# Kernel tuning notes

Measured on AMD Instinct MI355X. Metric: run time of the kernel, lower is better.

The kernel has to match this reference:

```python
import jax, jax.numpy as jnp
import numpy as np

LN_EPS = 1e-5
NEG_INF = -1e38


def wkv_scan(w, u, k, v):
    """Numerically-stable RWKV WKV recurrence (matches wkv_cuda forward).
    w: [C] (negative decay), u: [C] bonus, k/v: [B,T,C]. Returns y: [B,T,C]."""
    Bdim, T, C = k.shape

    def step(carry, kv_t):
        p, q, o = carry  # running num, den, log-scale, each [B,C]
        kt, vt = kv_t
        no = jnp.maximum(o, u + kt)
        A = jnp.exp(o - no)
        Bw = jnp.exp(u + kt - no)
        y = (A * p + Bw * vt) / (A * q + Bw)
        no2 = jnp.maximum(w + o, kt)
        A2 = jnp.exp(w + o - no2)
        B2 = jnp.exp(kt - no2)
        return (A2 * p + B2 * vt, A2 * q + B2, no2), y

    init = (jnp.zeros((Bdim, C), k.dtype), jnp.zeros((Bdim, C), k.dtype),
            jnp.full((Bdim, C), NEG_INF, k.dtype))
    kT = jnp.moveaxis(k, 1, 0)  # [T,B,C]
    vT = jnp.moveaxis(v, 1, 0)
    _, ys = jax.lax.scan(step, init, (kT, vT))
    return jnp.moveaxis(ys, 0, 1)  # [B,T,C]


def setup_inputs() -> dict:
    key = jax.random.key(0)
    ks = jax.random.split(key, 8)
    B, C, H, W = 16, 192, 56, 56
    s = 0.02
    x = jax.random.normal(ks[0], (B, C, H, W), jnp.float32)
    Wk = jax.random.normal(ks[1], (C, C), jnp.float32) * s
    Wv = jax.random.normal(ks[2], (C, C), jnp.float32) * s
    Wr = jax.random.normal(ks[3], (C, C), jnp.float32) * s
    Wo = jax.random.normal(ks[4], (C, C), jnp.float32) * s
    ln_g = jnp.ones((C,), jnp.float32)
    ln_b = jnp.zeros((C,), jnp.float32)
    w_decay = -6.0 + 0.1 * jax.random.normal(ks[5], (C,), jnp.float32)
    u = 0.1 * jax.random.normal(ks[6], (C,), jnp.float32)
    return {"x": x, "Wk": Wk, "Wv": Wv, "Wr": Wr, "Wo": Wo,
            "ln_g": ln_g, "ln_b": ln_b, "w_decay": w_decay, "u": u}


def reference(x, Wk, Wv, Wr, Wo, ln_g, ln_b, w_decay, u):
    B, C, H, W = x.shape
    xs = jnp.transpose(x.reshape(B, C, H * W), (0, 2, 1))  # [B,T,C]
    k = jnp.einsum('btc,dc->btd', xs, Wk)
    v = jnp.einsum('btc,dc->btd', xs, Wv)
    r = jnp.einsum('btc,dc->btd', xs, Wr)
    real_w = -jnp.exp(w_decay)
    x_fwd = wkv_scan(real_w, u, k, v)
    x_bwd = jnp.flip(wkv_scan(real_w, u, jnp.flip(k, 1), jnp.flip(v, 1)), 1)
    x_bi = 0.5 * (x_fwd + x_bwd)
    h = jax.nn.sigmoid(r) * x_bi
    mu = jnp.mean(h, axis=-1, keepdims=True)
    var = jnp.var(h, axis=-1, keepdims=True)
    h = (h - mu) * jax.lax.rsqrt(var + LN_EPS) * ln_g + ln_b
    out = jnp.einsum('btc,dc->btd', h, Wo)  # dropout is identity at eval
    return jnp.transpose(out, (0, 2, 1)).reshape(B, C, H, W)
```

## Files before the change

### kernel.cpp

```cpp
#include <hip/hip_runtime.h>
#include <hip/hip_bf16.h>

#define BB 16
#define CC 192
#define TPIX 3136
#define NCH 49
#define CHL 64
#define NNELE ((size_t)BB * TPIX * CC)
#define NSTATE ((size_t)2 * BB * NCH * CC)
#define WCH (CC * CC)

typedef __attribute__((ext_vector_type(8))) short bf16x8;
typedef __attribute__((ext_vector_type(4))) float f32x4;
typedef __attribute__((ext_vector_type(16))) float f32x16;

__device__ __forceinline__ unsigned short f2bf(float f) {
    __hip_bfloat16 b = __float2bfloat16(f);
    return *reinterpret_cast<unsigned short*>(&b);
}
__device__ __forceinline__ float bf2f(unsigned short h) {
    union { unsigned u; float f; } v; v.u = ((unsigned)h) << 16;
    return v.f;
}


__global__ __launch_bounds__(256) void wcvt_frag(
    const float* __restrict__ Wk, const float* __restrict__ Wv,
    const float* __restrict__ Wr, const float* __restrict__ Wo,
    unsigned short* __restrict__ wfrag)
{
    const int id = blockIdx.x * 256 + threadIdx.x;
    const int m = id / 4608;
    const int r = id % 4608;
    const int tile = r >> 6;
    const int lane = r & 63;
    const int dr = tile / 12, tk = tile % 12;
    const int d = dr * 32 + (lane & 31);
    const int c = tk * 16 + (lane >> 5) * 8;
    const float* W = (m == 0) ? Wk : (m == 1) ? Wv : (m == 2) ? Wr : Wo;
    const float4 a = *(const float4*)&W[d * CC + c];
    const float4 b = *(const float4*)&W[d * CC + c + 4];
    bf16x8 o;
    o[0] = (short)f2bf(a.x); o[1] = (short)f2bf(a.y);
    o[2] = (short)f2bf(a.z); o[3] = (short)f2bf(a.w);
    o[4] = (short)f2bf(b.x); o[5] = (short)f2bf(b.y);
    o[6] = (short)f2bf(b.z); o[7] = (short)f2bf(b.w);
    *(bf16x8*)&wfrag[(size_t)m * WCH + (size_t)tile * 512 + lane * 8] = o;
}

__global__ __launch_bounds__(256) void xcvt_frag(
    const float* __restrict__ x, unsigned short* __restrict__ xfrag)
{
    const int t0 = blockIdx.x * 32;
    const int b  = blockIdx.y;
    __shared__ float ls[CC][33];
    const int tid = threadIdx.x;
#pragma unroll
    for (int it = 0; it < 6; ++it) {
        const int c  = it * 32 + (tid >> 3);
        const int t4 = (tid & 7) * 4;
        *(float4*)&ls[c][t4] =
            *(const float4*)&x[((size_t)b * CC + c) * TPIX + t0 + t4];
    }
    __syncthreads();
    const size_t tbase = ((size_t)(b * TPIX + t0) >> 5) * 12;
#pragma unroll
    for (int it = 0; it < 3; ++it) {
        const int id = it * 256 + tid;
        const int tk = id >> 6;
        const int lane = id & 63;
        const int r32 = lane & 31;
        const int c0 = tk * 16 + (lane >> 5) * 8;
        bf16x8 o;
#pragma unroll
        for (int e = 0; e < 8; ++e)
            o[e] = (short)f2bf(ls[c0 + e][r32]);
        *(bf16x8*)&xfrag[(tbase + tk) * 512 + lane * 8] = o;
    }
}

__global__ __launch_bounds__(512, 4) void proj_mfma32(
    const unsigned short* __restrict__ xfrag,
    const unsigned short* __restrict__ wfrag,
    unsigned short* __restrict__ kbf, unsigned short* __restrict__ vbf,
    unsigned short* __restrict__ rfrag)
{
    __shared__ unsigned short wlds[WCH];
    const int tid  = threadIdx.x;
    const int lane = tid & 63;
    const int wv   = tid >> 6;
    const int tw   = wv >> 1;
    const int dwav = wv & 1;
    const int l31  = lane & 31;
    const int kh   = lane >> 5;
    const int m    = blockIdx.z;

    const size_t row0 = (size_t)blockIdx.x * 128 + tw * 32;
    const size_t xtb  = (row0 >> 5) * 12;

    bf16x8 xf[12];
#pragma unroll
    for (int ks = 0; ks < 12; ++ks)
        xf[ks] = *(const bf16x8*)&xfrag[(xtb + ks) * 512 + lane * 8];

    const unsigned short* wm = wfrag + (size_t)m * WCH;
#pragma unroll
    for (int it = 0; it < 9; ++it) {
        const int off = (it * 512 + tid) * 8;
        *(bf16x8*)&wlds[off] = *(const bf16x8*)&wm[off];
    }
    __syncthreads();

    f32x16 acc[3];
#pragma unroll
    for (int nn = 0; nn < 3; ++nn)
#pragma unroll
        for (int e = 0; e < 16; ++e) acc[nn][e] = 0.f;

#pragma unroll
    for (int ks = 0; ks < 12; ++ks) {
        bf16x8 wf[3];
#pragma unroll
        for (int nn = 0; nn < 3; ++nn)
            wf[nn] = *(const bf16x8*)&wlds[((dwav * 3 + nn) * 12 + ks) * 512 + lane * 8];
#pragma unroll
        for (int nn = 0; nn < 3; ++nn)
            acc[nn] = __builtin_amdgcn_mfma_f32_32x32x16_bf16(
                xf[ks], wf[nn], acc[nn], 0, 0, 0);
    }

    if (m == 2) {
#pragma unroll
        for (int nn = 0; nn < 3; ++nn) {
            const int d = dwav * 96 + nn * 32 + l31;
            const size_t tb = ((row0 >> 5) * 12 + (d >> 4)) * 512 +
                              (size_t)(((d >> 3) & 1) * 32) * 8 + (d & 7);
#pragma unroll
            for (int q = 0; q < 16; ++q) {
                const int tq = (q & 3) + 8 * (q >> 2) + 4 * kh;
                rfrag[tb + tq * 8] = f2bf(acc[nn][q]);
            }
        }
    } else {
        unsigned short* om = (m == 0) ? kbf : vbf;
#pragma unroll
        for (int nn = 0; nn < 3; ++nn) {
            const int d = dwav * 96 + nn * 32 + l31;
#pragma unroll
            for (int q = 0; q < 16; ++q) {
                const int t = (q & 3) + 8 * (q >> 2) + 4 * kh;
                om[(row0 + t) * CC + d] = f2bf(acc[nn][q]);
            }
        }
    }
}

__global__ __launch_bounds__(256) void wkv_chunk_kernel(
    const unsigned short* __restrict__ kb, const unsigned short* __restrict__ vb,
    const float* __restrict__ wdec,
    float* __restrict__ sp, float* __restrict__ sq, float* __restrict__ so)
{
    const int gid = blockIdx.x * 256 + threadIdx.x;
    const int c  = gid % CC;
    const int r  = gid / CC;
    const int ch = r % NCH;
    const int r2 = r / NCH;
    const int b  = r2 % BB;
    const int dir = r2 / BB;

    const float w = -__expf(wdec[c]);
    const int tstart = dir ? (TPIX - 1 - ch * CHL) : (ch * CHL);
    const long stride = dir ? -(long)CC : (long)CC;
    long idx = ((long)b * TPIX + tstart) * CC + c;

    float p = 0.f, q = 0.f, o = -1e38f;
#pragma unroll 4
    for (int j = 0; j < CHL; ++j) {
        const float kt = bf2f(kb[idx]), vt = bf2f(vb[idx]);
        const float wo  = w + o;
        const float no2 = fmaxf(wo, kt);
        const float A2  = __expf(wo - no2);
        const float B2  = __expf(kt - no2);
        p = A2 * p + B2 * vt;
        q = A2 * q + B2;
        o = no2;
        idx += stride;
    }
    sp[gid] = p; sq[gid] = q; so[gid] = o;
}

__global__ __launch_bounds__(256) void wkv_prefix_kernel(
    float* __restrict__ sp, float* __restrict__ sq, float* __restrict__ so,
    const float* __restrict__ wdec)
{
    const int tid = blockIdx.x * 256 + threadIdx.x;
    if (tid >= 2 * BB * CC) return;
    const int c = tid % CC;
    const int g = tid / CC;
    const float w  = -__expf(wdec[c]);
    const float wL = w * CHL;

    float P = 0.f, Q = 0.f, O = -1e38f;
    size_t idx = (size_t)g * NCH * CC + c;
    for (int ch = 0; ch < NCH; ++ch) {
        const float pl = sp[idx], ql = sq[idx], ol = so[idx];
        sp[idx] = P; sq[idx] = Q; so[idx] = O;
        const float Ow = O + wL;
        const float no = fmaxf(Ow, ol);
        const float A  = __expf(Ow - no);
        const float Bf = __expf(ol - no);
        P = A * P + Bf * pl;
        Q = A * Q + Bf * ql;
        O = no;
        idx += CC;
    }
}

__global__ __launch_bounds__(256) void wkv_emit_kernel(
    const unsigned short* __restrict__ kb, const unsigned short* __restrict__ vb,
    const float* __restrict__ wdec, const float* __restrict__ ubias,
    const float* __restrict__ sp, const float* __restrict__ sq,
    const float* __restrict__ so,
    unsigned short* __restrict__ yfwd, unsigned short* __restrict__ ybwd)
{
    const int gid = blockIdx.x * 256 + threadIdx.x;
    const int c  = gid % CC;
    const int r  = gid / CC;
    const int ch = r % NCH;
    const int r2 = r / NCH;
    const int b  = r2 % BB;
    const int dir = r2 / BB;

    const float w = -__expf(wdec[c]);
    const float u = ubias[c];
    const int tstart = dir ? (TPIX - 1 - ch * CHL) : (ch * CHL);
    const long stride = dir ? -(long)CC : (long)CC;
    const int rstep = dir ? -1 : 1;
    long idx = ((long)b * TPIX + tstart) * CC + c;
    long row = (long)b * TPIX + tstart;
    unsigned short* yout = dir ? ybwd : yfwd;
    const int ctile = c >> 4;
    const int clane = ((c >> 3) & 1) * 32;
    const int ce    = c & 7;

    float p = sp[gid], q = sq[gid], o = so[gid];
#pragma unroll 2
    for (int j = 0; j < CHL; ++j) {
        const float kt = bf2f(kb[idx]), vt = bf2f(vb[idx]);
        const float uk  = u + kt;
        const float no  = fmaxf(o, uk);
        const float A   = __expf(o - no);
        const float Bw  = __expf(uk - no);
        const float num = A * p + Bw * vt;
        const float den = A * q + Bw;
        const size_t off = ((size_t)(row >> 5) * 12 + ctile) * 512 +
                           (size_t)((row & 31) + clane) * 8 + ce;
        yout[off] = f2bf(0.5f * __fdividef(num, den));
        const float wo  = w + o;
        const float no2 = fmaxf(wo, kt);
        const float A2  = __expf(wo - no2);
        const float B2  = __expf(kt - no2);
        p = A2 * p + B2 * vt;
        q = A2 * q + B2;
        o = no2;
        idx += stride;
        row += rstep;
    }
}

__global__ __launch_bounds__(512, 2) void outproj_ln_mfma32(
    const unsigned short* __restrict__ yfwd, const unsigned short* __restrict__ ybwd,
    const unsigned short* __restrict__ rfrag,
    const float* __restrict__ gamma, const float* __restrict__ beta,
    const unsigned short* __restrict__ wo,
    float* __restrict__ out)
{
    __shared__ unsigned short wlds[WCH];
    __shared__ float gblds[CC];
    __shared__ float bblds[CC];
    const int tid  = threadIdx.x;
    const int lane = tid & 63;
    const int wv   = tid >> 6;
    const int tw   = wv >> 1;
    const int dwav = wv & 1;
    const int l31  = lane & 31;
    const int kh   = lane >> 5;

#pragma unroll
    for (int it = 0; it < 9; ++it) {
        const int off = (it * 512 + tid) * 8;
        *(bf16x8*)&wlds[off] = *(const bf16x8*)&wo[off];
    }
    if (tid < CC) { gblds[tid] = gamma[tid]; bblds[tid] = beta[tid]; }
    __syncthreads();

    const size_t row0 = (size_t)blockIdx.x * 128 + tw * 32;
    const size_t htb  = (row0 >> 5) * 12;

    bf16x8 hvb[12];
    float s = 0.f, s2 = 0.f;
#pragma unroll
    for (int ks = 0; ks < 12; ++ks) {
        const size_t fo = (htb + ks) * 512 + lane * 8;
        const bf16x8 yf = *(const bf16x8*)&yfwd[fo];
        const bf16x8 yb = *(const bf16x8*)&ybwd[fo];
        const bf16x8 rv = *(const bf16x8*)&rfrag[fo];
        bf16x8 hb;
#pragma unroll
        for (int e = 0; e < 8; ++e) {
            const float xb = bf2f((unsigned short)yf[e]) + bf2f((unsigned short)yb[e]);
            const float rr = bf2f((unsigned short)rv[e]);
            const float h  = xb / (1.f + __expf(-rr));
            s += h; s2 += h * h;
            hb[e] = (short)f2bf(h);
        }
        hvb[ks] = hb;
    }
    s  += __shfl_xor(s, 32);
    s2 += __shfl_xor(s2, 32);
    const float mu   = s * (1.f / CC);
    const float var  = s2 * (1.f / CC) - mu * mu;
    const float rstd = rsqrtf(var + 1e-5f);

#pragma unroll
    for (int ks = 0; ks < 12; ++ks) {
        const int cbase = ks * 16 + kh * 8;
        bf16x8 hb = hvb[ks];
#pragma unroll
        for (int e = 0; e < 8; ++e) {
            const float h = (bf2f((unsigned short)hb[e]) - mu) * rstd *
                            gblds[cbase + e] + bblds[cbase + e];
            hb[e] = (short)f2bf(h);
        }
        hvb[ks] = hb;
    }

    f32x16 acc[3];
#pragma unroll
    for (int nn = 0; nn < 3; ++nn)
#pragma unroll
        for (int e = 0; e < 16; ++e) acc[nn][e] = 0.f;

#pragma unroll
    for (int ks = 0; ks < 12; ++ks) {
        bf16x8 wf[3];
#pragma unroll
        for (int nn = 0; nn < 3; ++nn)
            wf[nn] = *(const bf16x8*)&wlds[((dwav * 3 + nn) * 12 + ks) * 512 + lane * 8];
#pragma unroll
        for (int nn = 0; nn < 3; ++nn)
            acc[nn] = __builtin_amdgcn_mfma_f32_32x32x16_bf16(
                hvb[ks], wf[nn], acc[nn], 0, 0, 0);
    }

#pragma unroll
    for (int nn = 0; nn < 3; ++nn) {
        const int d = dwav * 96 + nn * 32 + l31;
#pragma unroll
        for (int q2 = 0; q2 < 4; ++q2) {
            const size_t grow = row0 + 4 * kh + 8 * q2;
            const int b  = (int)(grow / TPIX);
            const int tl = (int)(grow % TPIX);
            f32x4 v4 = {acc[nn][q2 * 4 + 0], acc[nn][q2 * 4 + 1],
                        acc[nn][q2 * 4 + 2], acc[nn][q2 * 4 + 3]};
            *(f32x4*)&out[((size_t)b * CC + d) * TPIX + tl] = v4;
        }
    }
}

extern "C" void kernel_launch(void* const* d_in, const int* in_sizes, int n_in,
                              void* d_out, int out_size, void* d_ws, size_t ws_size,
                              hipStream_t stream)
{
    const float* x    = (const float*)d_in[0];
    const float* Wk   = (const float*)d_in[1];
    const float* Wv   = (const float*)d_in[2];
    const float* Wr   = (const float*)d_in[3];
    const float* Wo   = (const float*)d_in[4];
    const float* ln_g = (const float*)d_in[5];
    const float* ln_b = (const float*)d_in[6];
    const float* wdec = (const float*)d_in[7];
    const float* u    = (const float*)d_in[8];

    unsigned short* kbf   = (unsigned short*)d_ws;
    unsigned short* vbf   = kbf + NNELE;
    unsigned short* rfrag = vbf + NNELE;
    unsigned short* xfrag = rfrag + NNELE;
    unsigned short* wfrag = xfrag + NNELE;
    unsigned short* yfwd  = wfrag + 4 * WCH;
    unsigned short* ybwd  = yfwd + NNELE;
    float* sp = (float*)xfrag;
    float* sq = sp + NSTATE;
    float* so = sq + NSTATE;
    float* out = (float*)d_out;

    wcvt_frag<<<72, 256, 0, stream>>>(Wk, Wv, Wr, Wo, wfrag);
    xcvt_frag<<<dim3(TPIX / 32, BB), 256, 0, stream>>>(x, xfrag);

    proj_mfma32<<<dim3((BB * TPIX) / 128, 1, 3), 512, 0, stream>>>(
        xfrag, wfrag, kbf, vbf, rfrag);

    const int nth = (int)NSTATE;
    wkv_chunk_kernel<<<nth / 256, 256, 0, stream>>>(kbf, vbf, wdec, sp, sq, so);
    wkv_prefix_kernel<<<(2 * BB * CC + 255) / 256, 256, 0, stream>>>(sp, sq, so, wdec);
    wkv_emit_kernel<<<nth / 256, 256, 0, stream>>>(kbf, vbf, wdec, u, sp, sq, so, yfwd, ybwd);

    outproj_ln_mfma32<<<(BB * TPIX) / 128, 512, 0, stream>>>(
        yfwd, ybwd, rfrag, ln_g, ln_b, wfrag + 3 * WCH, out);
}
```

Baseline: 132.2 us.

## Fold LayerNorm into output projection via gamma-scaled weights and MFMA row sums

Rewrites LayerNorm plus the output projection algebraically. Gamma is folded into the bf16 Wo fragments, and Wo·gamma and Wo·beta are precomputed in a small new kernel. Per-row mean and variance are computed by extra MFMAs against a ones vector, and normalization is applied after the GEMM, so h is no longer held across two passes. This removes the 12-register-vector hvb buffer and the second normalization loop. In exchange it adds two extra MFMAs per k-step and an extra launch, and it computes variance from bf16-rounded h² via E[x²]-mu², which risks cancellation error. It also drops the min-2-blocks occupancy hint.

New measurement: 136.0 us. +2.8%, slower.

```diff
diff --git a/kernel.cpp b/kernel.cpp
--- a/kernel.cpp
+++ b/kernel.cpp
@@ -9,6 +9,7 @@
 #define NNELE ((size_t)BB * TPIX * CC)
 #define NSTATE ((size_t)2 * BB * NCH * CC)
 #define WCH (CC * CC)
+#define NROWS ((size_t)BB * TPIX)
 
 typedef __attribute__((ext_vector_type(8))) short bf16x8;
 typedef __attribute__((ext_vector_type(4))) float f32x4;
@@ -27,6 +28,7 @@
 __global__ __launch_bounds__(256) void wcvt_frag(
     const float* __restrict__ Wk, const float* __restrict__ Wv,
     const float* __restrict__ Wr, const float* __restrict__ Wo,
+    const float* __restrict__ gamma,
     unsigned short* __restrict__ wfrag)
 {
     const int id = blockIdx.x * 256 + threadIdx.x;
@@ -40,12 +42,32 @@
     const float* W = (m == 0) ? Wk : (m == 1) ? Wv : (m == 2) ? Wr : Wo;
     const float4 a = *(const float4*)&W[d * CC + c];
     const float4 b = *(const float4*)&W[d * CC + c + 4];
+    float g[8];
+#pragma unroll
+    for (int i = 0; i < 8; ++i) g[i] = (m == 3) ? gamma[c + i] : 1.f;
     bf16x8 o;
-    o[0] = (short)f2bf(a.x); o[1] = (short)f2bf(a.y);
-    o[2] = (short)f2bf(a.z); o[3] = (short)f2bf(a.w);
-    o[4] = (short)f2bf(b.x); o[5] = (short)f2bf(b.y);
-    o[6] = (short)f2bf(b.z); o[7] = (short)f2bf(b.w);
+    o[0] = (short)f2bf(a.x * g[0]); o[1] = (short)f2bf(a.y * g[1]);
+    o[2] = (short)f2bf(a.z * g[2]); o[3] = (short)f2bf(a.w * g[3]);
+    o[4] = (short)f2bf(b.x * g[4]); o[5] = (short)f2bf(b.y * g[5]);
+    o[6] = (short)f2bf(b.z * g[6]); o[7] = (short)f2bf(b.w * g[7]);
     *(bf16x8*)&wfrag[(size_t)m * WCH + (size_t)tile * 512 + lane * 8] = o;
+}
+
+__global__ __launch_bounds__(192) void wgb_kernel(
+    const float* __restrict__ Wo, const float* __restrict__ gamma,
+    const float* __restrict__ beta,
+    float* __restrict__ Wg, float* __restrict__ Wb)
+{
+    const int d = threadIdx.x;
+    float sg = 0.f, sb = 0.f;
+    for (int c = 0; c < CC; c += 4) {
+        const float4 w = *(const float4*)&Wo[d * CC + c];
+        const float4 g = *(const float4*)&gamma[c];
+        const float4 bb = *(const float4*)&beta[c];
+        sg += w.x * g.x + w.y * g.y + w.z * g.z + w.w * g.w;
+        sb += w.x * bb.x + w.y * bb.y + w.z * bb.z + w.w * bb.w;
+    }
+    Wg[d] = sg; Wb[d] = sb;
 }
 
 __global__ __launch_bounds__(256) void xcvt_frag(
@@ -268,16 +290,14 @@
     }
 }
 
-__global__ __launch_bounds__(512, 2) void outproj_ln_mfma32(
+__global__ __launch_bounds__(512) void outproj_ln_mfma32(
     const unsigned short* __restrict__ yfwd, const unsigned short* __restrict__ ybwd,
     const unsigned short* __restrict__ rfrag,
-    const float* __restrict__ gamma, const float* __restrict__ beta,
+    const float* __restrict__ Wg, const float* __restrict__ Wb,
     const unsigned short* __restrict__ wo,
     float* __restrict__ out)
 {
     __shared__ unsigned short wlds[WCH];
-    __shared__ float gblds[CC];
-    __shared__ float bblds[CC];
     const int tid  = threadIdx.x;
     const int lane = tid & 63;
     const int wv   = tid >> 6;
@@ -286,63 +306,43 @@
     const int l31  = lane & 31;
     const int kh   = lane >> 5;
 
+    const size_t row0 = (size_t)blockIdx.x * 128 + tw * 32;
+    const size_t htb  = (row0 >> 5) * 12;
+
 #pragma unroll
     for (int it = 0; it < 9; ++it) {
         const int off = (it * 512 + tid) * 8;
         *(bf16x8*)&wlds[off] = *(const bf16x8*)&wo[off];
     }
-    if (tid < CC) { gblds[tid] = gamma[tid]; bblds[tid] = beta[tid]; }
     __syncthreads();
 
-    const size_t row0 = (size_t)blockIdx.x * 128 + tw * 32;
-    const size_t htb  = (row0 >> 5) * 12;
-
-    bf16x8 hvb[12];
-    float s = 0.f, s2 = 0.f;
+    bf16x8 ones;
+#pragma unroll
+    for (int e = 0; e < 8; ++e) ones[e] = (short)0x3F80;
+
+    f32x16 acc[3], accs, accs2;
+#pragma unroll
+    for (int nn = 0; nn < 3; ++nn)
+#pragma unroll
+        for (int e = 0; e < 16; ++e) acc[nn][e] = 0.f;
+#pragma unroll
+    for (int e = 0; e < 16; ++e) { accs[e] = 0.f; accs2[e] = 0.f; }
+
 #pragma unroll
     for (int ks = 0; ks < 12; ++ks) {
         const size_t fo = (htb + ks) * 512 + lane * 8;
         const bf16x8 yf = *(const bf16x8*)&yfwd[fo];
         const bf16x8 yb = *(const bf16x8*)&ybwd[fo];
         const bf16x8 rv = *(const bf16x8*)&rfrag[fo];
-        bf16x8 hb;
+        bf16x8 hb, hq;
 #pragma unroll
         for (int e = 0; e < 8; ++e) {
             const float xb = bf2f((unsigned short)yf[e]) + bf2f((unsigned short)yb[e]);
             const float rr = bf2f((unsigned short)rv[e]);
-            const float h  = xb / (1.f + __expf(-rr));
-            s += h; s2 += h * h;
+            const float h  = __fdividef(xb, 1.f + __expf(-rr));
             hb[e] = (short)f2bf(h);
+            hq[e] = (short)f2bf(h * h);
         }
-        hvb[ks] = hb;
-    }
-    s  += __shfl_xor(s, 32);
-    s2 += __shfl_xor(s2, 32);
-    const float mu   = s * (1.f / CC);
-    const float var  = s2 * (1.f / CC) - mu * mu;
-    const float rstd = rsqrtf(var + 1e-5f);
-
-#pragma unroll
-    for (int ks = 0; ks < 12; ++ks) {
-        const int cbase = ks * 16 + kh * 8;
-        bf16x8 hb = hvb[ks];
-#pragma unroll
-        for (int e = 0; e < 8; ++e) {
-            const float h = (bf2f((unsigned short)hb[e]) - mu) * rstd *
-                            gblds[cbase + e] + bblds[cbase + e];
-            hb[e] = (short)f2bf(h);
-        }
-        hvb[ks] = hb;
-    }
-
-    f32x16 acc[3];
-#pragma unroll
-    for (int nn = 0; nn < 3; ++nn)
-#pragma unroll
-        for (int e = 0; e < 16; ++e) acc[nn][e] = 0.f;
-
-#pragma unroll
-    for (int ks = 0; ks < 12; ++ks) {
         bf16x8 wf[3];
 #pragma unroll
         for (int nn = 0; nn < 3; ++nn)
@@ -350,19 +350,36 @@
 #pragma unroll
         for (int nn = 0; nn < 3; ++nn)
             acc[nn] = __builtin_amdgcn_mfma_f32_32x32x16_bf16(
-                hvb[ks], wf[nn], acc[nn], 0, 0, 0);
+                hb, wf[nn], acc[nn], 0, 0, 0);
+        accs  = __builtin_amdgcn_mfma_f32_32x32x16_bf16(hb, ones, accs, 0, 0, 0);
+        accs2 = __builtin_amdgcn_mfma_f32_32x32x16_bf16(hq, ones, accs2, 0, 0, 0);
+    }
+
+    float muv[16], rsv[16];
+#pragma unroll
+    for (int q = 0; q < 16; ++q) {
+        const float mu  = accs[q] * (1.f / CC);
+        const float var = accs2[q] * (1.f / CC) - mu * mu;
+        muv[q] = mu;
+        rsv[q] = rsqrtf(var + 1e-5f);
     }
 
 #pragma unroll
     for (int nn = 0; nn < 3; ++nn) {
         const int d = dwav * 96 + nn * 32 + l31;
+        const float wg = Wg[d];
+        const float wb = Wb[d];
 #pragma unroll
         for (int q2 = 0; q2 < 4; ++q2) {
             const size_t grow = row0 + 4 * kh + 8 * q2;
             const int b  = (int)(grow / TPIX);
             const int tl = (int)(grow % TPIX);
-            f32x4 v4 = {acc[nn][q2 * 4 + 0], acc[nn][q2 * 4 + 1],
-                        acc[nn][q2 * 4 + 2], acc[nn][q2 * 4 + 3]};
+            f32x4 v4;
+#pragma unroll
+            for (int j = 0; j < 4; ++j) {
+                const int q = q2 * 4 + j;
+                v4[j] = rsv[q] * (acc[nn][q] - muv[q] * wg) + wb;
+            }
             *(f32x4*)&out[((size_t)b * CC + d) * TPIX + tl] = v4;
         }
     }
@@ -389,12 +406,15 @@
     unsigned short* wfrag = xfrag + NNELE;
     unsigned short* yfwd  = wfrag + 4 * WCH;
     unsigned short* ybwd  = yfwd + NNELE;
+    float* Wg_buf = (float*)(ybwd + NNELE);
+    float* Wb_buf = Wg_buf + CC;
     float* sp = (float*)xfrag;
     float* sq = sp + NSTATE;
     float* so = sq + NSTATE;
     float* out = (float*)d_out;
 
-    wcvt_frag<<<72, 256, 0, stream>>>(Wk, Wv, Wr, Wo, wfrag);
+    wcvt_frag<<<72, 256, 0, stream>>>(Wk, Wv, Wr, Wo, ln_g, wfrag);
+    wgb_kernel<<<1, 192, 0, stream>>>(Wo, ln_g, ln_b, Wg_buf, Wb_buf);
     xcvt_frag<<<dim3(TPIX / 32, BB), 256, 0, stream>>>(x, xfrag);
 
     proj_mfma32<<<dim3((BB * TPIX) / 128, 1, 3), 512, 0, stream>>>(
@@ -406,5 +426,5 @@
     wkv_emit_kernel<<<nth / 256, 256, 0, stream>>>(kbf, vbf, wdec, u, sp, sq, so, yfwd, ybwd);
 
     outproj_ln_mfma32<<<(BB * TPIX) / 128, 512, 0, stream>>>(
-        yfwd, ybwd, rfrag, ln_g, ln_b, wfrag + 3 * WCH, out);
-}
+        yfwd, ybwd, rfrag, Wg_buf, Wb_buf, wfrag + 3 * WCH, out);
+}
```
